# Kernel tuning notes

Hardware: AMD Instinct MI355X
Metric: run time of the kernel (lower is better)

## Reference

```python
import jax, jax.numpy as jnp
import numpy as np
from jax import lax

# Heston model constants (from init_kwargs)
N_STEPS = 512
T = 1.0
V0 = 0.235 ** 2
KAPPA = 1.0
THETA = 0.04
SIGMA_V = 2.0
RHO = -0.7
S0 = 100.0
DT = T / N_STEPS
SQRT_DT = DT ** 0.5
RHO_PERP = (1.0 - RHO * RHO) ** 0.5

BATCH = 65536


def setup_inputs() -> dict:
    key = jax.random.key(0)
    k1, k2 = jax.random.split(key)
    Z_vol = jax.random.normal(k1, (BATCH, N_STEPS, 2), dtype=jnp.float32)
    Z_price = jax.random.normal(k2, (BATCH, N_STEPS), dtype=jnp.float32)
    return {"Z_vol": Z_vol, "Z_price": Z_price}


def reference(Z_vol, Z_price):
    dtype = Z_vol.dtype
    batch = Z_price.shape[0]
    dt = jnp.asarray(DT, dtype)
    sqrt_dt = jnp.asarray(SQRT_DT, dtype)

    # time-major noise for scan: [n_steps, batch]
    Zv = jnp.transpose(Z_vol[:, :, 0])
    Zp = jnp.transpose(Z_price)

    def step(V_k, zs):
        zv, zp = zs
        V_pos = jnp.maximum(V_k, 0.0)  # full truncation
        V_next = V_k + KAPPA * (THETA - V_pos) * dt + SIGMA_V * jnp.sqrt(V_pos * dt) * zv
        V_next = jnp.maximum(V_next, 0.0)
        dB = RHO * sqrt_dt * zv + RHO_PERP * sqrt_dt * zp  # correlated Brownian increment
        log_inc = -0.5 * V_pos * dt + jnp.sqrt(V_pos) * dB
        return V_next, (V_next, log_inc)

    V_init = jnp.full((batch,), V0, dtype=dtype)
    _, (V_path, log_incs) = lax.scan(step, V_init, (Zv, Zp))

    # V: [batch, n_steps+1]
    V = jnp.concatenate([V_init[:, None], jnp.transpose(V_path)], axis=1)
    # cumulative log-price, prepend 0
    log_S = jnp.concatenate(
        [jnp.zeros((batch, 1), dtype=dtype), jnp.cumsum(jnp.transpose(log_incs), axis=1)],
        axis=1,
    )
    S = S0 * jnp.exp(log_S)
    return S, V
```

## Files before the change

kernel.cpp:

```cpp
#include <hip/hip_runtime.h>

#define NSTEPS 512
#define BATCH  65536

#define C_DT       (1.0f / 512.0f)
#define C_SQRT_DT  0.04419417382415922f
#define C_RHO      (-0.7f)
#define C_RHOPERP  0.7141428428542850f
#define C_V0       0.055225f
#define C_THETA    0.04f
#define C_SIGMAV   2.0f
#define C_S0       100.0f

__global__ __launch_bounds__(256) void heston_paths(
    const float* __restrict__ Zvol,
    const float* __restrict__ Zp,
    float* __restrict__ S,
    float* __restrict__ V)
{
    const int b = blockIdx.x * blockDim.x + threadIdx.x;

    const float4* __restrict__ zv4 = (const float4*)(Zvol + (size_t)b * (NSTEPS * 2));
    const float4* __restrict__ zp4 = (const float4*)(Zp   + (size_t)b * NSTEPS);
    float* __restrict__ Srow = S + (size_t)b * (NSTEPS + 1);
    float* __restrict__ Vrow = V + (size_t)b * (NSTEPS + 1);

    float v    = C_V0;
    float logS = 0.0f;

    Srow[0] = C_S0;
    Vrow[0] = C_V0;

    for (int k = 0; k < NSTEPS; k += 8) {
        const int q = k >> 1;
        float4 a0 = zv4[q + 0];
        float4 a1 = zv4[q + 1];
        float4 a2 = zv4[q + 2];
        float4 a3 = zv4[q + 3];
        float4 p0 = zp4[(k >> 2) + 0];
        float4 p1 = zp4[(k >> 2) + 1];

        float zv[8] = {a0.x, a0.z, a1.x, a1.z, a2.x, a2.z, a3.x, a3.z};
        float zp[8] = {p0.x, p0.y, p0.z, p0.w, p1.x, p1.y, p1.z, p1.w};

        float sOut[8], vOut[8];
        #pragma unroll
        for (int j = 0; j < 8; ++j) {
            const float vpos  = fmaxf(v, 0.0f);
            float vnext = v + (C_THETA - vpos) * C_DT
                            + C_SIGMAV * sqrtf(vpos * C_DT) * zv[j];
            vnext = fmaxf(vnext, 0.0f);
            const float dB = C_RHO * C_SQRT_DT * zv[j] + C_RHOPERP * C_SQRT_DT * zp[j];
            logS += -0.5f * vpos * C_DT + sqrtf(vpos) * dB;
            sOut[j] = C_S0 * __expf(logS);
            vOut[j] = vnext;
            v = vnext;
        }

        #pragma unroll
        for (int j = 0; j < 8; ++j) {
            Srow[k + 1 + j] = sOut[j];
            Vrow[k + 1 + j] = vOut[j];
        }
    }
}

extern "C" void kernel_launch(void* const* d_in, const int* in_sizes, int n_in,
                              void* d_out, int out_size, void* d_ws, size_t ws_size,
                              hipStream_t stream) {
    const float* Zvol = (const float*)d_in[0];
    const float* Zp   = (const float*)d_in[1];
    float* S = (float*)d_out;
    float* V = S + (size_t)BATCH * (NSTEPS + 1);

    heston_paths<<<BATCH / 256, 256, 0, stream>>>(Zvol, Zp, S, V);
}
```

Measured before the change: 725.6 us.

## Stage outputs through LDS tiles for coalesced transposed stores

Each 64-thread block now writes its per-step S and V values into padded shared-memory tiles of 64 paths by 64 steps. After each tile it stores them so that consecutive lanes write consecutive steps of the same path row, replacing the old pattern where each thread wrote its own row and the lanes of a wave were strided far apart in memory. Block size drops from 256 to 64 threads, one wave per block, so only wave-level barriers are needed. The cost is 33 KB of LDS per block, which limits occupancy, and the noise loads are still strided per thread.

```diff
diff --git a/kernel.cpp b/kernel.cpp
--- a/kernel.cpp
+++ b/kernel.cpp
@@ -2,6 +2,9 @@
 
 #define NSTEPS 512
 #define BATCH  65536
+#define NOUT   (NSTEPS + 1)
+#define TILE   64
+#define PAD    65
 
 #define C_DT       (1.0f / 512.0f)
 #define C_SQRT_DT  0.04419417382415922f
@@ -12,56 +15,70 @@
 #define C_SIGMAV   2.0f
 #define C_S0       100.0f
 
-__global__ __launch_bounds__(256) void heston_paths(
+__global__ __launch_bounds__(64) void heston_paths(
     const float* __restrict__ Zvol,
     const float* __restrict__ Zp,
     float* __restrict__ S,
     float* __restrict__ V)
 {
-    const int b = blockIdx.x * blockDim.x + threadIdx.x;
+    __shared__ float St[64][PAD];
+    __shared__ float Vt[64][PAD];
+
+    const int lane     = threadIdx.x;
+    const int pathBase = blockIdx.x * 64;
+    const int b        = pathBase + lane;
 
     const float4* __restrict__ zv4 = (const float4*)(Zvol + (size_t)b * (NSTEPS * 2));
     const float4* __restrict__ zp4 = (const float4*)(Zp   + (size_t)b * NSTEPS);
-    float* __restrict__ Srow = S + (size_t)b * (NSTEPS + 1);
-    float* __restrict__ Vrow = V + (size_t)b * (NSTEPS + 1);
 
     float v    = C_V0;
     float logS = 0.0f;
 
-    Srow[0] = C_S0;
-    Vrow[0] = C_V0;
+    S[(size_t)b * NOUT] = C_S0;
+    V[(size_t)b * NOUT] = C_V0;
 
-    for (int k = 0; k < NSTEPS; k += 8) {
-        const int q = k >> 1;
-        float4 a0 = zv4[q + 0];
-        float4 a1 = zv4[q + 1];
-        float4 a2 = zv4[q + 2];
-        float4 a3 = zv4[q + 3];
-        float4 p0 = zp4[(k >> 2) + 0];
-        float4 p1 = zp4[(k >> 2) + 1];
+    for (int k0 = 0; k0 < NSTEPS; k0 += TILE) {
+        #pragma unroll
+        for (int kk = 0; kk < TILE; kk += 8) {
+            const int k = k0 + kk;
+            const int q = k >> 1;
+            float4 a0 = zv4[q + 0];
+            float4 a1 = zv4[q + 1];
+            float4 a2 = zv4[q + 2];
+            float4 a3 = zv4[q + 3];
+            float4 p0 = zp4[(k >> 2) + 0];
+            float4 p1 = zp4[(k >> 2) + 1];
 
-        float zv[8] = {a0.x, a0.z, a1.x, a1.z, a2.x, a2.z, a3.x, a3.z};
-        float zp[8] = {p0.x, p0.y, p0.z, p0.w, p1.x, p1.y, p1.z, p1.w};
+            float zv[8] = {a0.x, a0.z, a1.x, a1.z, a2.x, a2.z, a3.x, a3.z};
+            float zp[8] = {p0.x, p0.y, p0.z, p0.w, p1.x, p1.y, p1.z, p1.w};
 
-        float sOut[8], vOut[8];
-        #pragma unroll
-        for (int j = 0; j < 8; ++j) {
-            const float vpos  = fmaxf(v, 0.0f);
-            float vnext = v + (C_THETA - vpos) * C_DT
-                            + C_SIGMAV * sqrtf(vpos * C_DT) * zv[j];
-            vnext = fmaxf(vnext, 0.0f);
-            const float dB = C_RHO * C_SQRT_DT * zv[j] + C_RHOPERP * C_SQRT_DT * zp[j];
-            logS += -0.5f * vpos * C_DT + sqrtf(vpos) * dB;
-            sOut[j] = C_S0 * __expf(logS);
-            vOut[j] = vnext;
-            v = vnext;
+            #pragma unroll
+            for (int j = 0; j < 8; ++j) {
+                const float vpos  = fmaxf(v, 0.0f);
+                float vnext = v + (C_THETA - vpos) * C_DT
+                                + C_SIGMAV * sqrtf(vpos * C_DT) * zv[j];
+                vnext = fmaxf(vnext, 0.0f);
+                const float dB = C_RHO * C_SQRT_DT * zv[j]
+                               + C_RHOPERP * C_SQRT_DT * zp[j];
+                logS += -0.5f * vpos * C_DT + sqrtf(vpos) * dB;
+                St[lane][kk + j] = C_S0 * __expf(logS);
+                Vt[lane][kk + j] = vnext;
+                v = vnext;
+            }
         }
 
-        #pragma unroll
-        for (int j = 0; j < 8; ++j) {
-            Srow[k + 1 + j] = sOut[j];
-            Vrow[k + 1 + j] = vOut[j];
+        asm volatile("s_waitcnt lgkmcnt(0)" ::: "memory");
+        __builtin_amdgcn_wave_barrier();
+
+        const size_t outBase = (size_t)pathBase * NOUT + 1 + k0 + lane;
+        #pragma unroll 8
+        for (int r = 0; r < 64; ++r) {
+            S[outBase + (size_t)r * NOUT] = St[r][lane];
+            V[outBase + (size_t)r * NOUT] = Vt[r][lane];
         }
+
+        asm volatile("s_waitcnt lgkmcnt(0)" ::: "memory");
+        __builtin_amdgcn_wave_barrier();
     }
 }
 
@@ -71,7 +88,7 @@
     const float* Zvol = (const float*)d_in[0];
     const float* Zp   = (const float*)d_in[1];
     float* S = (float*)d_out;
-    float* V = S + (size_t)BATCH * (NSTEPS + 1);
+    float* V = S + (size_t)BATCH * NOUT;
 
-    heston_paths<<<BATCH / 256, 256, 0, stream>>>(Zvol, Zp, S, V);
+    heston_paths<<<BATCH / 64, 64, 0, stream>>>(Zvol, Zp, S, V);
 }
```

After: 624.3 us. 1.16x faster.
